# Kernel optimization log

Measured on AMD Instinct MI355X. Metric: run time of the kernel, lower is better.

## Reference

```python
import jax, jax.numpy as jnp
import numpy as np
from jax import lax

V = 30000   # vocab (input_types)
D = 512     # model_dim
H = D // 2  # per-direction LSTM hidden
R = 64      # relation_types
B = 32      # batch
T = 512     # seq len
E = 64      # max entities
L = 2       # lstm layers


def setup_inputs() -> dict:
    key = jax.random.key(0)
    ks = jax.random.split(key, 12)
    s = 0.02
    sents = jax.random.randint(ks[0], (B, T), 0, V, dtype=jnp.int64)
    # ent_inds[b, k] = (ent_id, start, end); -1 sentinel marks padding
    ids = np.tile(np.arange(E), (B, 1))
    starts = ids * 8
    ends = starts + 4  # 4-token spans, max end = 63*8+4 = 508 <= T
    ent = np.stack([ids, starts, ends], axis=-1).astype(np.int64)
    for b in range(1, B, 2):
        ent[b, E - 8:] = -1  # ragged: odd batches have 56 entities
    ent_inds = jnp.asarray(ent)
    emb = jax.random.normal(ks[1], (V, D), jnp.float32) * s
    Wih = jax.random.normal(ks[2], (L, 2, 4 * H, D), jnp.float32) * s
    Whh = jax.random.normal(ks[3], (L, 2, 4 * H, H), jnp.float32) * s
    bih = jnp.zeros((L, 2, 4 * H), jnp.float32)
    bhh = jnp.zeros((L, 2, 4 * H), jnp.float32)
    ln_g = jnp.ones((D,), jnp.float32)
    ln_b = jnp.zeros((D,), jnp.float32)
    rel1_w = jax.random.normal(ks[4], (D, D), jnp.float32) * s
    rel1_b = jnp.zeros((D,), jnp.float32)
    rel2_w = jax.random.normal(ks[5], (D, D), jnp.float32) * s
    rel2_b = jnp.zeros((D,), jnp.float32)
    proj_w = jax.random.normal(ks[6], (D, D), jnp.float32) * s
    proj_b = jnp.zeros((D,), jnp.float32)
    dec_w = jax.random.normal(ks[7], (R, D), jnp.float32) * s
    dec_b = jnp.zeros((R,), jnp.float32)
    return dict(sents=sents, ent_inds=ent_inds, max_ents=E, emb=emb,
                Wih=Wih, Whh=Whh, bih=bih, bhh=bhh, ln_g=ln_g, ln_b=ln_b,
                rel1_w=rel1_w, rel1_b=rel1_b, rel2_w=rel2_w, rel2_b=rel2_b,
                proj_w=proj_w, proj_b=proj_b, dec_w=dec_w, dec_b=dec_b)


def _lstm_dir(x, Wih, Whh, bih, bhh, reverse):
    # x: [B, T, Din] -> [B, T, H]; PyTorch gate order i, f, g, o
    xs = jnp.swapaxes(x, 0, 1)  # [T, B, Din]
    bsz = xs.shape[1]
    h0 = jnp.zeros((bsz, Whh.shape[1]), x.dtype)
    c0 = jnp.zeros_like(h0)

    def step(carry, xt):
        h, c = carry
        z = xt @ Wih.T + h @ Whh.T + bih + bhh
        i, f, g, o = jnp.split(z, 4, axis=-1)
        c = jax.nn.sigmoid(f) * c + jax.nn.sigmoid(i) * jnp.tanh(g)
        h = jax.nn.sigmoid(o) * jnp.tanh(c)
        return (h, c), h

    _, ys = lax.scan(step, (h0, c0), xs, reverse=reverse)
    return jnp.swapaxes(ys, 0, 1)


def _bilstm(x, Wih, Whh, bih, bhh):
    for l in range(L):
        fwd = _lstm_dir(x, Wih[l, 0], Whh[l, 0], bih[l, 0], bhh[l, 0], False)
        bwd = _lstm_dir(x, Wih[l, 1], Whh[l, 1], bih[l, 1], bhh[l, 1], True)
        x = jnp.concatenate([fwd, bwd], axis=-1)
    return x


def _forward(sents, ent_inds, max_ents, emb, Wih, Whh, bih, bhh, ln_g, ln_b,
             rel1_w, rel1_b, rel2_w, rel2_b, proj_w, proj_b, dec_w, dec_b):
    x = emb[sents]                                   # [B,T,D]
    x = _bilstm(x, Wih, Whh, bih, bhh)               # [B,T,D]
    bs, _, hd = x.shape
    # ragged span mean-pool via inclusive prefix sums
    csum = jnp.concatenate([jnp.zeros((bs, 1, hd), x.dtype),
                            jnp.cumsum(x, axis=1)], axis=1)  # [B,T+1,D]
    ids, st, en = ent_inds[..., 0], ent_inds[..., 1], ent_inds[..., 2]
    valid = ids >= 0                                 # [B,E]
    sid = jnp.where(valid, ids, 0)
    sst = jnp.where(valid, st, 0)
    sen = jnp.where(valid, en, 1)
    b_idx = jnp.arange(bs)[:, None]
    seg_sum = csum[b_idx, sen] - csum[b_idx, sst]    # [B,E,D]
    length = jnp.maximum(sen - sst, 1).astype(x.dtype)
    means = jnp.where(valid[..., None], seg_sum / length[..., None], 0.0)
    cont = jnp.zeros((bs, max_ents, hd), x.dtype).at[b_idx, sid].add(means)
    mask = jnp.zeros((bs, max_ents), x.dtype).at[b_idx, sid].add(
        valid.astype(x.dtype))
    mask = jnp.clip(mask, 0.0, 1.0)
    # LayerNorm
    mu = jnp.mean(cont, axis=-1, keepdims=True)
    var = jnp.var(cont, axis=-1, keepdims=True)
    cw = (cont - mu) / jnp.sqrt(var + 1e-5) * ln_g + ln_b
    rel1 = cw @ rel1_w.T + rel1_b                    # [B,E,D]
    rel2 = cw @ rel2_w.T + rel2_b                    # [B,E,D]
    out = jax.nn.relu(rel1[:, None, :, :] + rel2[:, :, None, :])  # [B,E,E,D]
    out = jax.nn.relu(out @ proj_w.T + proj_b)
    out = out @ dec_w.T + dec_b                      # [B,E,E,R]
    out = out * mask[:, :, None, None] * mask[:, None, :, None]
    return jax.nn.log_softmax(out, axis=-1)


def reference(sents, ent_inds, max_ents, emb, Wih, Whh, bih, bhh, ln_g, ln_b,
              rel1_w, rel1_b, rel2_w, rel2_b, proj_w, proj_b, dec_w, dec_b):
    return _forward(sents, ent_inds, max_ents, emb, Wih, Whh, bih, bhh,
                    ln_g, ln_b, rel1_w, rel1_b, rel2_w, rel2_b,
                    proj_w, proj_b, dec_w, dec_b)
```

## Files before the change

### kernel.cpp

```cpp
#include <hip/hip_runtime.h>

typedef unsigned short u16;
typedef unsigned int u32;

#define Bsz 32
#define Tlen 512
#define Dm 512
#define Hh 256
#define G4 1024
#define Ee 64
#define Rr 64
#define BT 16384
#define BE 2048

using bshort8 = __attribute__((ext_vector_type(8))) short;
using f32x16  = __attribute__((ext_vector_type(16))) float;
using i32x4   = __attribute__((ext_vector_type(4))) int;
#define MFMA32(a, b, c) __builtin_amdgcn_mfma_f32_32x32x16_bf16(a, b, c, 0, 0, 0)
#define MFMAI8(a, b, c) __builtin_amdgcn_mfma_i32_16x16x64_i8(a, b, c, 0, 0, 0)

__device__ __forceinline__ float b2f(u16 v) {
    union { u32 u; float f; } x; x.u = ((u32)v) << 16; return x.f;
}
__device__ __forceinline__ u16 f2b(float f) {
    union { float f; u32 u; } x; x.f = f;
    u32 r = (x.u + 0x7fffu + ((x.u >> 16) & 1u)) >> 16;
    return (u16)r;
}
__device__ __forceinline__ u32 pk2(float a, float b) {
    return (u32)f2b(a) | ((u32)f2b(b) << 16);
}
__device__ __forceinline__ bool is_bf16_mode(const u32* flagp) {
    return *flagp == 0x3F803F80u;
}
__device__ __forceinline__ float fsig(float x) {
    return __builtin_amdgcn_rcpf(1.f + __expf(-x));
}
__device__ __forceinline__ float ftanh(float x) {
    return 1.f - 2.f * __builtin_amdgcn_rcpf(1.f + __expf(2.f * x));
}
__device__ __forceinline__ float hsc_from(int bits) {
    float p = __int_as_float(bits);
    return p > 0.f ? fminf(2.f * p, 1.f) : 1.f;
}
__device__ __forceinline__ void sync_lds_only() {
    asm volatile("s_waitcnt lgkmcnt(0)" ::: "memory");
    __builtin_amdgcn_s_barrier();
}

struct Ptr10 { const void* p[10]; };
__global__ __launch_bounds__(256) void cvt_fused(Ptr10 srcs, float* __restrict__ dst,
        const u32* __restrict__ flagp) {
    bool bf = is_bf16_mode(flagp);
    int i = blockIdx.x * 256 + threadIdx.x;
    if (i >= 535104) return;
    const int off[10] = {0, 4096, 8192, 8704, 9216, 271360,
                         271872, 534016, 534528, 535040};
    int seg = 0;
#pragma unroll
    for (int k = 1; k < 10; ++k) seg += (i >= off[k]) ? 1 : 0;
    int local = i - off[seg];
    const void* s = srcs.p[seg];
    dst[i] = bf ? b2f(((const u16*)s)[local]) : ((const float*)s)[local];
}

__global__ __launch_bounds__(256) void cvtb_any(const void* __restrict__ src,
        u16* __restrict__ dst, int n, const u32* __restrict__ flagp) {
    bool bf = is_bf16_mode(flagp);
    int i = blockIdx.x * 256 + threadIdx.x;
    if (i >= n) return;
    dst[i] = bf ? ((const u16*)src)[i] : f2b(((const float*)src)[i]);
}

__global__ __launch_bounds__(256) void cvtb4_kernel(const float* __restrict__ src,
        u16* __restrict__ dst, int n4) {
    int i = blockIdx.x * 256 + threadIdx.x;
    if (i >= n4) return;
    float4 v = ((const float4*)src)[i];
    ushort4 o;
    o.x = f2b(v.x); o.y = f2b(v.y); o.z = f2b(v.z); o.w = f2b(v.w);
    ((ushort4*)dst)[i] = o;
}

__global__ __launch_bounds__(256) void whh_quant(const void* __restrict__ whh,
        signed char* __restrict__ qw, float* __restrict__ wsc,
        const u32* __restrict__ flagp) {
    bool bf = is_bf16_mode(flagp);
    int row = blockIdx.x * 4 + (threadIdx.x >> 6);
    int l = threadIdx.x & 63;
    long base = (long)row * 256 + l * 4;
    float v0, v1, v2, v3;
    if (bf) {
        ushort4 uv = *(const ushort4*)((const u16*)whh + base);
        v0 = b2f(uv.x); v1 = b2f(uv.y); v2 = b2f(uv.z); v3 = b2f(uv.w);
    } else {
        float4 fv = *(const float4*)((const float*)whh + base);
        v0 = fv.x; v1 = fv.y; v2 = fv.z; v3 = fv.w;
    }
    float m = fmaxf(fmaxf(fabsf(v0), fabsf(v1)), fmaxf(fabsf(v2), fabsf(v3)));
#pragma unroll
    for (int mk = 32; mk > 0; mk >>= 1) m = fmaxf(m, __shfl_xor(m, mk));
    float inv = m > 0.f ? 127.f / m : 0.f;
    int q0 = (int)rintf(fminf(fmaxf(v0 * inv, -127.f), 127.f));
    int q1 = (int)rintf(fminf(fmaxf(v1 * inv, -127.f), 127.f));
    int q2 = (int)rintf(fminf(fmaxf(v2 * inv, -127.f), 127.f));
    int q3 = (int)rintf(fminf(fmaxf(v3 * inv, -127.f), 127.f));
    u32 pk = (u32)(q0 & 255) | ((u32)(q1 & 255) << 8) |
             ((u32)(q2 & 255) << 16) | ((u32)(q3 & 255) << 24);
    ((u32*)qw)[row * 64 + l] = pk;
    if (l == 0) wsc[row] = m * (1.f / 127.f);
}

__global__ __launch_bounds__(256) void embed_kernel(const int* __restrict__ sents,
        const void* __restrict__ emb, float* __restrict__ x, const u32* __restrict__ flagp) {
    bool bf = is_bf16_mode(flagp);
    int i = blockIdx.x * 256 + threadIdx.x;
    int tok = i >> 7, c4 = (i & 127) * 4;
    long base = (long)sents[tok] * Dm + c4;
    float4 o;
    if (bf) {
        ushort4 uv = *(const ushort4*)((const u16*)emb + base);
        o = make_float4(b2f(uv.x), b2f(uv.y), b2f(uv.z), b2f(uv.w));
    } else {
        o = *(const float4*)((const float*)emb + base);
    }
    *(float4*)(x + (long)tok * Dm + c4) = o;
}

__global__ __launch_bounds__(256) void gemm_nt(const float* __restrict__ A,
        const float* __restrict__ W, const float* __restrict__ b1, const float* __restrict__ b2,
        float* __restrict__ C, int M, int N, int K,
        long wStride, long bStride, long cStride) {
    __shared__ float As[16][132];
    __shared__ float Ws[16][132];
    int z = blockIdx.z;
    const float* Wz = W + (long)z * wStride;
    float* Cz = C + (long)z * cStride;
    int m0 = blockIdx.y * 128, n0 = blockIdx.x * 128;
    int t = threadIdx.x, ty = t >> 4, tx = t & 15;

    float bias[8];
#pragma unroll
    for (int j = 0; j < 8; ++j) {
        int n = n0 + tx * 8 + j;
        float bb = 0.f;
        if (b1) bb += b1[z * bStride + n];
        if (b2) bb += b2[z * bStride + n];
        bias[j] = bb;
    }
    float acc[8][8] = {};
    int lrow = t >> 2, lkq = (t & 3) * 4;
    for (int k0 = 0; k0 < K; k0 += 16) {
        __syncthreads();
#pragma unroll
        for (int h = 0; h < 2; ++h) {
            int row = lrow + h * 64;
            float4 av = *(const float4*)&A[(long)(m0 + row) * K + k0 + lkq];
            As[lkq + 0][row] = av.x; As[lkq + 1][row] = av.y;
            As[lkq + 2][row] = av.z; As[lkq + 3][row] = av.w;
            float4 wv = *(const float4*)&Wz[(long)(n0 + row) * K + k0 + lkq];
            Ws[lkq + 0][row] = wv.x; Ws[lkq + 1][row] = wv.y;
            Ws[lkq + 2][row] = wv.z; Ws[lkq + 3][row] = wv.w;
        }
        __syncthreads();
#pragma unroll
        for (int k = 0; k < 16; ++k) {
            float4 a0 = *(const float4*)&As[k][ty * 8];
            float4 a1 = *(const float4*)&As[k][ty * 8 + 4];
            float4 w0 = *(const float4*)&Ws[k][tx * 8];
            float4 w1 = *(const float4*)&Ws[k][tx * 8 + 4];
            float av8[8] = {a0.x,a0.y,a0.z,a0.w,a1.x,a1.y,a1.z,a1.w};
            float wv8[8] = {w0.x,w0.y,w0.z,w0.w,w1.x,w1.y,w1.z,w1.w};
#pragma unroll
            for (int i = 0; i < 8; ++i)
#pragma unroll
                for (int j = 0; j < 8; ++j)
                    acc[i][j] += av8[i] * wv8[j];
        }
    }
#pragma unroll
    for (int i = 0; i < 8; ++i) {
        long m = m0 + ty * 8 + i;
#pragma unroll
        for (int jq = 0; jq < 2; ++jq) {
            int n = n0 + tx * 8 + jq * 4;
            float4 o;
            o.x = acc[i][jq*4+0] + bias[jq*4+0];
            o.y = acc[i][jq*4+1] + bias[jq*4+1];
            o.z = acc[i][jq*4+2] + bias[jq*4+2];
            o.w = acc[i][jq*4+3] + bias[jq*4+3];
            *(float4*)&Cz[m * N + n] = o;
        }
    }
}

__global__ __launch_bounds__(256, 2) void gemm_mfma(const u16* __restrict__ A,
        const u16* __restrict__ W, const float* __restrict__ b1, const float* __restrict__ b2,
        float* __restrict__ C, int M, int N, int K,
        long wStride, long bStride, long cStride) {
    __shared__ u16 As[4 * 128 * 8];
    __shared__ u16 Bs[4 * 128 * 8];
    int z = blockIdx.z;
    const u16* Wz = W + (long)z * wStride;
    float* Cz = C + (long)z * cStride;
    int m0 = blockIdx.y * 128, n0 = blockIdx.x * 128;
    int t = threadIdx.x;
    int w = t >> 6, l = t & 63, ln31 = l & 31, lk = l >> 5;
    int mh = (w >> 1) * 64, nh = (w & 1) * 64;
    f32x16 acc[2][2];
#pragma unroll
    for (int i = 0; i < 2; ++i)
#pragma unroll
        for (int j = 0; j < 2; ++j)
#pragma unroll
            for (int r = 0; r < 16; ++r) acc[i][j][r] = 0.f;

    int srow = t >> 1, skb = (t & 1) * 2;
    const u16* Arow = A + (long)(m0 + srow) * K + skb * 8;
    const u16* Wrow = Wz + (long)(n0 + srow) * K + skb * 8;
    for (int k0 = 0; k0 < K; k0 += 32) {
        __syncthreads();
        uint4 a0 = *(const uint4*)(Arow + k0);
        uint4 a1 = *(const uint4*)(Arow + k0 + 8);
        uint4 b0 = *(const uint4*)(Wrow + k0);
        uint4 b1v = *(const uint4*)(Wrow + k0 + 8);
        *(uint4*)(As + ((skb * 128 + srow) << 3)) = a0;
        *(uint4*)(As + (((skb + 1) * 128 + srow) << 3)) = a1;
        *(uint4*)(Bs + ((skb * 128 + srow) << 3)) = b0;
        *(uint4*)(Bs + (((skb + 1) * 128 + srow) << 3)) = b1v;
        __syncthreads();
#pragma unroll
        for (int ks = 0; ks < 2; ++ks) {
            int kb = ks * 2 + lk;
            bshort8 av0 = *(const bshort8*)(As + ((kb * 128 + mh + ln31) << 3));
            bshort8 av1 = *(const bshort8*)(As + ((kb * 128 + mh + 32 + ln31) << 3));
            bshort8 bv0 = *(const bshort8*)(Bs + ((kb * 128 + nh + ln31) << 3));
            bshort8 bv1 = *(const bshort8*)(Bs + ((kb * 128 + nh + 32 + ln31) << 3));
            acc[0][0] = MFMA32(av0, bv0, acc[0][0]);
            acc[0][1] = MFMA32(av0, bv1, acc[0][1]);
            acc[1][0] = MFMA32(av1, bv0, acc[1][0]);
            acc[1][1] = MFMA32(av1, bv1, acc[1][1]);
        }
    }
#pragma unroll
    for (int j = 0; j < 2; ++j) {
        int n = n0 + nh + j * 32 + ln31;
        float bb = 0.f;
        if (b1) bb += b1[z * bStride + n];
        if (b2) bb += b2[z * bStride + n];
#pragma unroll
        for (int i = 0; i < 2; ++i) {
            long mb = m0 + mh + i * 32 + 4 * lk;
#pragma unroll
            for (int r = 0; r < 16; ++r) {
                long mrow = mb + (r & 3) + 8 * (r >> 2);
                Cz[mrow * N + n] = acc[i][j][r] + bb;
            }
        }
    }
}

__global__ __attribute__((amdgpu_flat_work_group_size(512, 512)))
__attribute__((amdgpu_waves_per_eu(2, 2)))
void lstm_scan_i8(
        const float* __restrict__ xp, const signed char* __restrict__ qw,
        const float* __restrict__ wsc, float* __restrict__ y) {
    __shared__ u32 h8[2][64];
    __shared__ int hmx[4];
    int bid = blockIdx.x;
    int dir = bid & 1, b = bid >> 1;
    int t = threadIdx.x, w = t >> 6, l = t & 63;
    int ln15 = l & 15, lk4 = l >> 4;
    int e8 = ln15 & 7;
    int u = w * 32 + lk4 * 8 + e8;
    bool wr = (ln15 < 8);

    i32x4 wf[8][4];
    {
        int q = ln15 >> 2, j = ln15 & 3;
        const signed char* rp = qw + ((long)dir << 18)
            + ((long)(j * 256 + w * 32 + q * 8) << 8) + lk4 * 16;
#pragma unroll
        for (int e = 0; e < 8; ++e)
#pragma unroll
            for (int ks = 0; ks < 4; ++ks)
                wf[e][ks] = *(const i32x4*)(rp + ((long)e << 8) + ks * 64);
    }
#pragma unroll
    for (int e = 0; e < 8; ++e)
#pragma unroll
        for (int ks = 0; ks < 4; ++ks)
            asm volatile("" : "+v"(wf[e][ks]));

    float scg0, scg1, scg2, scg3;
    {
        const float* wl = wsc + (dir << 10);
        scg0 = wl[u]       * (1.f / 127.f);
        scg1 = wl[256 + u] * (1.f / 127.f);
        scg2 = wl[512 + u] * (1.f / 127.f);
        scg3 = wl[768 + u] * (1.f / 127.f);
    }
    const float* xpb = xp + (long)dir * BT * G4 + ((long)b << 19);
    float c = 0.f, am = 0.f;
    float xq0, xq1, xq2, xq3;
    {
        int tt0 = dir ? 511 : 0;
        const float* xr = xpb + ((long)tt0 << 10) + u;
        xq0 = xr[0]; xq1 = xr[256]; xq2 = xr[512]; xq3 = xr[768];
    }
    if (t < 64) h8[0][t] = 0u;
    if (t < 4) hmx[t] = 0;
    __syncthreads();

#pragma unroll 1
    for (int s = 0; s < Tlen; ++s) {
        int tt = dir ? (511 - s) : s;
        int p = s & 1;
        float hrec  = hsc_from(hmx[(s + 3) & 3]);
        float usedq = hsc_from(hmx[s & 3]);
        i32x4 bv0 = *(const i32x4*)((const char*)h8[p] + 0 * 64 + lk4 * 16);
        i32x4 bv1 = *(const i32x4*)((const char*)h8[p] + 1 * 64 + lk4 * 16);
        i32x4 bv2 = *(const i32x4*)((const char*)h8[p] + 2 * 64 + lk4 * 16);
        i32x4 bv3 = *(const i32x4*)((const char*)h8[p] + 3 * 64 + lk4 * 16);
        float nx0 = 0.f, nx1 = 0.f, nx2 = 0.f, nx3 = 0.f;
        if (s < 511) {
            int tn = dir ? (510 - s) : (s + 1);
            const float* xr = xpb + ((long)tn << 10) + u;
            nx0 = xr[0]; nx1 = xr[256]; nx2 = xr[512]; nx3 = xr[768];
        }
        i32x4 acc[8];
#pragma unroll
        for (int e = 0; e < 8; ++e) {
            acc[e][0] = 0; acc[e][1] = 0; acc[e][2] = 0; acc[e][3] = 0;
        }
#pragma unroll
        for (int e = 0; e < 8; ++e) {
            acc[e] = MFMAI8(wf[e][0], bv0, acc[e]);
            acc[e] = MFMAI8(wf[e][1], bv1, acc[e]);
            acc[e] = MFMAI8(wf[e][2], bv2, acc[e]);
            acc[e] = MFMAI8(wf[e][3], bv3, acc[e]);
        }
        {
            float amr = fmaxf(am, __shfl_xor(am, 32));
            amr = fmaxf(amr, __shfl_xor(amr, 16));
            amr = fmaxf(amr, __shfl_xor(amr, 4));
            amr = fmaxf(amr, __shfl_xor(amr, 2));
            amr = fmaxf(amr, __shfl_xor(amr, 1));
            if (l == 0) atomicMax(&hmx[(s + 1) & 3], __float_as_int(amr));
            if (t == 0) hmx[(s + 2) & 3] = 0;
        }
        i32x4 t0 = (e8 & 1) ? acc[1] : acc[0];
        i32x4 t1 = (e8 & 1) ? acc[3] : acc[2];
        i32x4 t2 = (e8 & 1) ? acc[5] : acc[4];
        i32x4 t3 = (e8 & 1) ? acc[7] : acc[6];
        i32x4 u0 = (e8 & 2) ? t1 : t0;
        i32x4 u1 = (e8 & 2) ? t3 : t2;
        i32x4 zv = (e8 & 4) ? u1 : u0;
        float zi = (float)zv[0] * (scg0 * hrec) + xq0;
        float zf = (float)zv[1] * (scg1 * hrec) + xq1;
        float zg = (float)zv[2] * (scg2 * hrec) + xq2;
        float zo = (float)zv[3] * (scg3 * hrec) + xq3;
        c = fsig(zf) * c + fsig(zi) * ftanh(zg);
        float h = fsig(zo) * ftanh(c);
        if (wr)
            y[(((long)((b << 9) + tt)) << 9) + (dir << 8) + u] = h;
        int qi = (int)rintf(fminf(fmaxf(h * (127.f / usedq), -127.f), 127.f));
        if (wr)
            ((signed char*)h8[p ^ 1])[u] = (signed char)qi;
        am = fabsf(h);
        xq0 = nx0; xq1 = nx1; xq2 = nx2; xq3 = nx3;
        sync_lds_only();
    }
}

__global__ __launch_bounds__(128) void pool_kernel(const float* __restrict__ y,
        const int* __restrict__ ent, float* __restrict__ cont, float* __restrict__ mask) {
    int be = blockIdx.x, b = be >> 6;
    int id = ent[be * 3], st = ent[be * 3 + 1], en = ent[be * 3 + 2];
    if (id < 0 || id >= Ee) return;
    int len = en - st; if (len < 1) len = 1;
    float inv = 1.f / (float)len;
    int t = threadIdx.x;
    for (int d = t; d < Dm; d += 128) {
        float s = 0.f;
        for (int q = st; q < en; ++q) s += y[((long)b * Tlen + q) * Dm + d];
        atomicAdd(&cont[((long)b * Ee + id) * Dm + d], s * inv);
    }
    if (t == 0) atomicAdd(&mask[b * Ee + id], 1.f);
}

__global__ __launch_bounds__(256) void ln_kernel(const float* __restrict__ cont,
        const float* __restrict__ g, const float* __restrict__ bta, float* __restrict__ cw) {
    __shared__ float red[256];
    int be = blockIdx.x, t = threadIdx.x;
    const float* xr = cont + (long)be * Dm;
    float v0 = xr[t], v1 = xr[t + 256];
    red[t] = v0 + v1;
    __syncthreads();
#pragma unroll
    for (int o = 128; o > 0; o >>= 1) {
        if (t < o) red[t] += red[t + o];
        __syncthreads();
    }
    float mu = red[0] * (1.f / 512.f);
    __syncthreads();
    float d0 = v0 - mu, d1 = v1 - mu;
    red[t] = d0 * d0 + d1 * d1;
    __syncthreads();
#pragma unroll
    for (int o = 128; o > 0; o >>= 1) {
        if (t < o) red[t] += red[t + o];
        __syncthreads();
    }
    float rs = rsqrtf(red[0] * (1.f / 512.f) + 1e-5f);
    cw[(long)be * Dm + t]       = d0 * rs * g[t] + bta[t];
    cw[(long)be * Dm + t + 256] = d1 * rs * g[t + 256] + bta[t + 256];
}

__global__ __launch_bounds__(256, 2) void pair_head_mfma(
        const float* __restrict__ r1o, const float* __restrict__ r2o,
        const u16* __restrict__ pwB, const float* __restrict__ proj_b,
        const u16* __restrict__ dwB, const float* __restrict__ dec_b,
        const float* __restrict__ mask, void* __restrict__ outv,
        const u32* __restrict__ flagp) {
    __shared__ u16 Ub[64 * 64 * 8];
    __shared__ float red[256];
    float* lg = (float*)Ub;
    int bid = blockIdx.x, b = bid >> 6;
    int t = threadIdx.x;
    int w = t >> 6, l = t & 63, ln31 = l & 31, lk = l >> 5;
    bool bf = is_bf16_mode(flagp);

    {
        int m = t & 63, kseg = t >> 6;
        const float* r1r = r1o + ((long)b * Ee + m) * Dm + kseg * 128;
        const float* r2r = r2o + (long)bid * Dm + kseg * 128;
#pragma unroll
        for (int q = 0; q < 16; ++q) {
            float4 x0 = *(const float4*)(r1r + q * 8);
            float4 x1 = *(const float4*)(r1r + q * 8 + 4);
            float4 y0 = *(const float4*)(r2r + q * 8);
            float4 y1 = *(const float4*)(r2r + q * 8 + 4);
            uint4 o;
            o.x = pk2(fmaxf(x0.x + y0.x, 0.f), fmaxf(x0.y + y0.y, 0.f));
            o.y = pk2(fmaxf(x0.z + y0.z, 0.f), fmaxf(x0.w + y0.w, 0.f));
            o.z = pk2(fmaxf(x1.x + y1.x, 0.f), fmaxf(x1.y + y1.y, 0.f));
            o.w = pk2(fmaxf(x1.z + y1.z, 0.f), fmaxf(x1.w + y1.w, 0.f));
            int kb = kseg * 16 + q;
            *(uint4*)(Ub + (((kb << 6) + m) << 3)) = o;
        }
    }
    __syncthreads();

    f32x16 acc[2][4];
#pragma unroll
    for (int i = 0; i < 2; ++i)
#pragma unroll
        for (int j = 0; j < 4; ++j)
#pragma unroll
            for (int r = 0; r < 16; ++r) acc[i][j][r] = 0.f;
    const u16* pwW = pwB + (long)(w * 128) * Dm;
#pragma unroll 1
    for (int ks = 0; ks < 32; ++ks) {
        int kb = ks * 2 + lk;
        bshort8 a0 = *(const bshort8*)(Ub + (((kb << 6) + ln31) << 3));
        bshort8 a1 = *(const bshort8*)(Ub + (((kb << 6) + 32 + ln31) << 3));
#pragma unroll
        for (int nt = 0; nt < 4; ++nt) {
            bshort8 bv = *(const bshort8*)(pwW + (long)(nt * 32 + ln31) * Dm
                                           + ks * 16 + lk * 8);
            acc[0][nt] = MFMA32(a0, bv, acc[0][nt]);
            acc[1][nt] = MFMA32(a1, bv, acc[1][nt]);
        }
    }
    __syncthreads();

#pragma unroll
    for (int nt = 0; nt < 4; ++nt) {
        int n = w * 128 + nt * 32 + ln31;
        float pb = proj_b[n];
        int kbp = n >> 3, ni = n & 7;
#pragma unroll
        for (int i = 0; i < 2; ++i) {
#pragma unroll
            for (int r = 0; r < 16; ++r) {
                int m = i * 32 + (r & 3) + 8 * (r >> 2) + 4 * lk;
                Ub[(((kbp << 6) + m) << 3) + ni] = f2b(fmaxf(acc[i][nt][r] + pb, 0.f));
            }
        }
    }
    __syncthreads();

    f32x16 acc2;
#pragma unroll
    for (int r = 0; r < 16; ++r) acc2[r] = 0.f;
    int mt = w >> 1, nt2 = w & 1;
#pragma unroll 1
    for (int ks = 0; ks < 32; ++ks) {
        int kb = ks * 2 + lk;
        bshort8 a = *(const bshort8*)(Ub + (((kb << 6) + mt * 32 + ln31) << 3));
        bshort8 bv = *(const bshort8*)(dwB + (long)(nt2 * 32 + ln31) * Dm
                                       + ks * 16 + lk * 8);
        acc2 = MFMA32(a, bv, acc2);
    }
    __syncthreads();

    float mx = fminf(mask[bid], 1.f);
    {
        int r = nt2 * 32 + ln31;
        float db = dec_b[r];
#pragma unroll
        for (int rg = 0; rg < 16; ++rg) {
            int yy = mt * 32 + (rg & 3) + 8 * (rg >> 2) + 4 * lk;
            float my = fminf(mask[b * Ee + yy], 1.f);
            lg[yy * 68 + r] = (acc2[rg] + db) * mx * my;
        }
    }
    __syncthreads();

    {
        int yy = t >> 2, part = t & 3;
        float m = -1e30f;
#pragma unroll
        for (int q = 0; q < 16; ++q) m = fmaxf(m, lg[yy * 68 + part * 16 + q]);
        red[t] = m;
        __syncthreads();
        float m4 = fmaxf(fmaxf(red[yy * 4], red[yy * 4 + 1]),
                         fmaxf(red[yy * 4 + 2], red[yy * 4 + 3]));
        __syncthreads();
        float ssum = 0.f;
#pragma unroll
        for (int q = 0; q < 16; ++q) ssum += expf(lg[yy * 68 + part * 16 + q] - m4);
        red[t] = ssum;
        __syncthreads();
        float lse = m4 + logf(red[yy * 4] + red[yy * 4 + 1] + red[yy * 4 + 2] + red[yy * 4 + 3]);
        long obase = ((long)bid * 64 + yy) * 64;
        if (bf) {
            u16* o16 = (u16*)outv;
#pragma unroll
            for (int q = 0; q < 16; ++q)
                o16[obase + part * 16 + q] = f2b(lg[yy * 68 + part * 16 + q] - lse);
        } else {
            float* o32 = (float*)outv;
#pragma unroll
            for (int q = 0; q < 16; ++q)
                o32[obase + part * 16 + q] = lg[yy * 68 + part * 16 + q] - lse;
        }
    }
}

extern "C" void kernel_launch(void* const* d_in, const int* in_sizes, int n_in,
                              void* d_out, int out_size, void* d_ws, size_t ws_size,
                              hipStream_t stream) {
    (void)in_sizes; (void)n_in; (void)out_size; (void)ws_size;
    const int* sents = (const int*)d_in[0];
    const int* ent   = (const int*)d_in[1];
    const void* emb  = d_in[3];
    const void* Wih  = d_in[4];
    const void* Whh  = d_in[5];
    const void* bih  = d_in[6];
    const void* bhh  = d_in[7];
    const u32* flagp = (const u32*)d_in[8];

    float* ws = (float*)d_ws;
    float* bufA = ws;
    float* bufB = bufA + (long)BT * Dm;
    float* xp   = bufB + (long)BT * Dm;
    float* fWhh = xp + 2L * BT * G4;
    float* cont = fWhh + 4L * G4 * Hh;
    float* maskp= cont + (long)BE * Dm;
    float* cw   = maskp + BE;
    float* r1   = cw + (long)BE * Dm;
    float* r2   = r1 + (long)BE * Dm;
    float* fbih = r2 + (long)BE * Dm;
    float* fbhh = fbih + 4L * G4;
    float* flng = fbhh + 4L * G4;
    float* flnb = flng + Dm;
    float* fr1w = flnb + Dm;
    float* fr1b = fr1w + (long)Dm * Dm;
    float* fr2w = fr1b + Dm;
    float* fr2b = fr2w + (long)Dm * Dm;
    float* fpb  = fr2b + Dm;
    float* fdb  = fpb + Dm;
    u16* wihB = (u16*)(fdb + Rr);
    u16* pwB  = wihB + 4L * G4 * Dm;
    u16* dwB  = pwB + (long)Dm * Dm;

    signed char* qwhh = (signed char*)fWhh;
    float* wscA = (float*)(qwhh + (4L * G4 * Hh));
    u16* xb = (u16*)cont;

    Ptr10 ps;
    ps.p[0] = bih;      ps.p[1] = bhh;      ps.p[2] = d_in[8];  ps.p[3] = d_in[9];
    ps.p[4] = d_in[10]; ps.p[5] = d_in[11]; ps.p[6] = d_in[12]; ps.p[7] = d_in[13];
    ps.p[8] = d_in[15]; ps.p[9] = d_in[17];
    cvt_fused<<<(535104 + 255) / 256, 256, 0, stream>>>(ps, fbih, flagp);
    whh_quant<<<1024, 256, 0, stream>>>(Whh, qwhh, wscA, flagp);
    cvtb_any<<<(4 * G4 * Dm) / 256, 256, 0, stream>>>(Wih, wihB, 4 * G4 * Dm, flagp);
    cvtb_any<<<(Dm * Dm) / 256, 256, 0, stream>>>(d_in[14], pwB, Dm * Dm, flagp);
    cvtb_any<<<(Rr * Dm) / 256, 256, 0, stream>>>(d_in[16], dwB, Rr * Dm, flagp);

    embed_kernel<<<(BT * Dm / 4) / 256, 256, 0, stream>>>(sents, emb, bufA, flagp);

    float* lin = bufA; float* lout = bufB;
    for (int l = 0; l < 2; ++l) {
        cvtb4_kernel<<<(BT * Dm / 4) / 256, 256, 0, stream>>>(lin, xb, BT * Dm / 4);
        gemm_mfma<<<dim3(G4 / 128, BT / 128, 2), 256, 0, stream>>>(
            xb, wihB + (long)l * 2 * G4 * Dm, fbih + l * 2 * G4, fbhh + l * 2 * G4,
            xp, BT, G4, Dm, (long)G4 * Dm, (long)G4, (long)BT * G4);
        lstm_scan_i8<<<64, 512, 0, stream>>>(xp, qwhh + (long)l * 2 * G4 * Hh,
                                             wscA + l * 2 * G4, lout);
        float* tmp = lin; lin = lout; lout = tmp;
    }
    hipMemsetAsync(cont, 0, ((long)BE * Dm + BE) * sizeof(float), stream);
    pool_kernel<<<BE, 128, 0, stream>>>(lin, ent, cont, maskp);
    ln_kernel<<<BE, 256, 0, stream>>>(cont, flng, flnb, cw);
    gemm_nt<<<dim3(Dm / 128, BE / 128, 1), 256, 0, stream>>>(cw, fr1w, fr1b, nullptr,
            r1, BE, Dm, Dm, 0, 0, 0);
    gemm_nt<<<dim3(Dm / 128, BE / 128, 1), 256, 0, stream>>>(cw, fr2w, fr2b, nullptr,
            r2, BE, Dm, Dm, 0, 0, 0);
    pair_head_mfma<<<BE, 256, 0, stream>>>(r1, r2, pwB, fpb, dwB, fdb, maskp,
                                           d_out, flagp);
}
```

Before: 1.744 ms.

## Process two batch sequences per LSTM scan block to share resident weights

Each LSTM scan workgroup now advances two batch sequences of the same direction in lockstep, so the grid shrinks from 64 to 32 blocks. Each sequence keeps its own h8 buffers and scale state, while the quantized recurrent weights stay in registers and serve both. The aim is to overlap the two independent recurrence chains within each step and share one LDS barrier per step, hiding MFMA and activation latency in this latency-bound serial loop. The cost is roughly double the work per step per block, higher register pressure, and fewer active CUs.

Result: slower. 2.589 ms (+48.4%).

```diff
diff --git a/kernel.cpp b/kernel.cpp
--- a/kernel.cpp
+++ b/kernel.cpp
@@ -265,10 +265,11 @@
 void lstm_scan_i8(
         const float* __restrict__ xp, const signed char* __restrict__ qw,
         const float* __restrict__ wsc, float* __restrict__ y) {
-    __shared__ u32 h8[2][64];
-    __shared__ int hmx[4];
+    __shared__ u32 h8[2][2][64];
+    __shared__ int hmx[2][4];
     int bid = blockIdx.x;
-    int dir = bid & 1, b = bid >> 1;
+    int dir = bid & 1;
+    int bA = (bid >> 1) << 1, bB = bA | 1;
     int t = threadIdx.x, w = t >> 6, l = t & 63;
     int ln15 = l & 15, lk4 = l >> 4;
     int e8 = ln15 & 7;
@@ -300,28 +301,30 @@
         scg2 = wl[512 + u] * (1.f / 127.f);
         scg3 = wl[768 + u] * (1.f / 127.f);
     }
-    const float* xpb = xp + (long)dir * BT * G4 + ((long)b << 19);
-    float c = 0.f, am = 0.f;
-    float xq0, xq1, xq2, xq3;
+    const float* xpbA = xp + (long)dir * BT * G4 + ((long)bA << 19);
+    const float* xpbB = xp + (long)dir * BT * G4 + ((long)bB << 19);
+    float cA = 0.f, cB = 0.f, amA = 0.f, amB = 0.f;
+    float xqA[4], xqB[4];
     {
         int tt0 = dir ? 511 : 0;
-        const float* xr = xpb + ((long)tt0 << 10) + u;
-        xq0 = xr[0]; xq1 = xr[256]; xq2 = xr[512]; xq3 = xr[768];
-    }
-    if (t < 64) h8[0][t] = 0u;
-    if (t < 4) hmx[t] = 0;
-    __syncthreads();
-
-#pragma unroll 1
-    for (int s = 0; s < Tlen; ++s) {
-        int tt = dir ? (511 - s) : s;
-        int p = s & 1;
-        float hrec  = hsc_from(hmx[(s + 3) & 3]);
-        float usedq = hsc_from(hmx[s & 3]);
-        i32x4 bv0 = *(const i32x4*)((const char*)h8[p] + 0 * 64 + lk4 * 16);
-        i32x4 bv1 = *(const i32x4*)((const char*)h8[p] + 1 * 64 + lk4 * 16);
-        i32x4 bv2 = *(const i32x4*)((const char*)h8[p] + 2 * 64 + lk4 * 16);
-        i32x4 bv3 = *(const i32x4*)((const char*)h8[p] + 3 * 64 + lk4 * 16);
+        const float* xrA = xpbA + ((long)tt0 << 10) + u;
+        xqA[0] = xrA[0]; xqA[1] = xrA[256]; xqA[2] = xrA[512]; xqA[3] = xrA[768];
+        const float* xrB = xpbB + ((long)tt0 << 10) + u;
+        xqB[0] = xrB[0]; xqB[1] = xrB[256]; xqB[2] = xrB[512]; xqB[3] = xrB[768];
+    }
+    if (t < 64) { h8[0][0][t] = 0u; h8[1][0][t] = 0u; }
+    if (t < 4) { hmx[0][t] = 0; hmx[1][t] = 0; }
+    __syncthreads();
+
+    auto do_seq = [&](u32 (*h8s)[64], int* hmxs, const float* xpb,
+                      float& c, float& am, float (&xq)[4], int b,
+                      int s, int tt, int p) {
+        float hrec  = hsc_from(hmxs[(s + 3) & 3]);
+        float usedq = hsc_from(hmxs[s & 3]);
+        i32x4 bv0 = *(const i32x4*)((const char*)h8s[p] + 0 * 64 + lk4 * 16);
+        i32x4 bv1 = *(const i32x4*)((const char*)h8s[p] + 1 * 64 + lk4 * 16);
+        i32x4 bv2 = *(const i32x4*)((const char*)h8s[p] + 2 * 64 + lk4 * 16);
+        i32x4 bv3 = *(const i32x4*)((const char*)h8s[p] + 3 * 64 + lk4 * 16);
         float nx0 = 0.f, nx1 = 0.f, nx2 = 0.f, nx3 = 0.f;
         if (s < 511) {
             int tn = dir ? (510 - s) : (s + 1);
@@ -346,8 +349,8 @@
             amr = fmaxf(amr, __shfl_xor(amr, 4));
             amr = fmaxf(amr, __shfl_xor(amr, 2));
             amr = fmaxf(amr, __shfl_xor(amr, 1));
-            if (l == 0) atomicMax(&hmx[(s + 1) & 3], __float_as_int(amr));
-            if (t == 0) hmx[(s + 2) & 3] = 0;
+            if (l == 0) atomicMax(&hmxs[(s + 1) & 3], __float_as_int(amr));
+            if (t == 0) hmxs[(s + 2) & 3] = 0;
         }
         i32x4 t0 = (e8 & 1) ? acc[1] : acc[0];
         i32x4 t1 = (e8 & 1) ? acc[3] : acc[2];
@@ -356,19 +359,27 @@
         i32x4 u0 = (e8 & 2) ? t1 : t0;
         i32x4 u1 = (e8 & 2) ? t3 : t2;
         i32x4 zv = (e8 & 4) ? u1 : u0;
-        float zi = (float)zv[0] * (scg0 * hrec) + xq0;
-        float zf = (float)zv[1] * (scg1 * hrec) + xq1;
-        float zg = (float)zv[2] * (scg2 * hrec) + xq2;
-        float zo = (float)zv[3] * (scg3 * hrec) + xq3;
+        float zi = (float)zv[0] * (scg0 * hrec) + xq[0];
+        float zf = (float)zv[1] * (scg1 * hrec) + xq[1];
+        float zg = (float)zv[2] * (scg2 * hrec) + xq[2];
+        float zo = (float)zv[3] * (scg3 * hrec) + xq[3];
         c = fsig(zf) * c + fsig(zi) * ftanh(zg);
         float h = fsig(zo) * ftanh(c);
         if (wr)
             y[(((long)((b << 9) + tt)) << 9) + (dir << 8) + u] = h;
         int qi = (int)rintf(fminf(fmaxf(h * (127.f / usedq), -127.f), 127.f));
         if (wr)
-            ((signed char*)h8[p ^ 1])[u] = (signed char)qi;
+            ((signed char*)h8s[p ^ 1])[u] = (signed char)qi;
         am = fabsf(h);
-        xq0 = nx0; xq1 = nx1; xq2 = nx2; xq3 = nx3;
+        xq[0] = nx0; xq[1] = nx1; xq[2] = nx2; xq[3] = nx3;
+    };
+
+#pragma unroll 1
+    for (int s = 0; s < Tlen; ++s) {
+        int tt = dir ? (511 - s) : s;
+        int p = s & 1;
+        do_seq(h8[0], hmx[0], xpbA, cA, amA, xqA, bA, s, tt, p);
+        do_seq(h8[1], hmx[1], xpbB, cB, amB, xqB, bB, s, tt, p);
         sync_lds_only();
     }
 }
@@ -608,7 +619,7 @@
         gemm_mfma<<<dim3(G4 / 128, BT / 128, 2), 256, 0, stream>>>(
             xb, wihB + (long)l * 2 * G4 * Dm, fbih + l * 2 * G4, fbhh + l * 2 * G4,
             xp, BT, G4, Dm, (long)G4 * Dm, (long)G4, (long)BT * G4);
-        lstm_scan_i8<<<64, 512, 0, stream>>>(xp, qwhh + (long)l * 2 * G4 * Hh,
+        lstm_scan_i8<<<32, 512, 0, stream>>>(xp, qwhh + (long)l * 2 * G4 * Hh,
                                              wscA + l * 2 * G4, lout);
         float* tmp = lin; lin = lout; lout = tmp;
     }
```
